# Performance work log

Measured on AMD Instinct MI355X. Metric: run time of the kernel, lower is better.

Reference implementation:

```python
import jax, jax.numpy as jnp
import numpy as np

V = 50000; C0 = 2000; C1 = 10000   # vocab and adaptive-softmax cutoffs
E = 512; H = 1024; B = 32; T = 128
H1 = H // 4; H2 = H // 16           # div_val = 4.0 per source formula
S1 = C1 - C0; S2 = V - C1


def setup_inputs() -> dict:
    key = jax.random.key(0)
    ks = jax.random.split(key, 12)
    # lengths sorted descending, max length == T (required by output.view(b*(T-1),-1))
    lengths = jnp.sort(jax.random.randint(ks[0], (B,), T // 2, T + 1))[::-1]
    lengths = lengths.at[0].set(T).astype(jnp.int64)
    x = jax.random.randint(ks[1], (B, T), 1, V)
    x = jnp.where(jnp.arange(T)[None, :] < lengths[:, None], x, 0).astype(jnp.int64)  # PAD=0 beyond length
    emb = (jax.random.normal(ks[2], (V, E), jnp.float32) * 0.02).at[0].set(0.0)  # padding_idx=0
    w_ih = jax.random.normal(ks[3], (3 * H, E), jnp.float32) * 0.02
    w_hh = jax.random.normal(ks[4], (3 * H, H), jnp.float32) * 0.02
    b_ih = jnp.zeros((3 * H,), jnp.float32)
    b_hh = jnp.zeros((3 * H,), jnp.float32)
    head_w = jax.random.normal(ks[5], (C0 + 2, H), jnp.float32) * 0.02   # shortlist + 2 cluster logits
    p1 = jax.random.normal(ks[6], (H1, H), jnp.float32) * 0.02
    t1 = jax.random.normal(ks[7], (S1, H1), jnp.float32) * 0.02
    p2 = jax.random.normal(ks[8], (H2, H), jnp.float32) * 0.02
    t2 = jax.random.normal(ks[9], (S2, H2), jnp.float32) * 0.02
    hidden = jnp.zeros((1, B, H), jnp.float32)
    return dict(x=x, lengths=lengths, hidden=hidden, emb=emb, w_ih=w_ih, w_hh=w_hh,
                b_ih=b_ih, b_hh=b_hh, head_w=head_w, p1=p1, t1=t1, p2=p2, t2=t2)


def gru_masked(inp, h0, w_ih, w_hh, b_ih, b_hh, lengths):
    """Torch GRU on packed sequence of lengths-1: frozen hidden + zero outputs past length."""
    xp = jnp.einsum('bte,ge->btg', inp, w_ih) + b_ih  # [B, T-1, 3H] input projections

    def step(h, args):
        xpt, t = args
        hp = h @ w_hh.T + b_hh
        xr, xz, xn = jnp.split(xpt, 3, axis=-1)
        hr, hz, hn = jnp.split(hp, 3, axis=-1)
        r = jax.nn.sigmoid(xr + hr)
        z = jax.nn.sigmoid(xz + hz)
        n = jnp.tanh(xn + r * hn)
        h_new = (1.0 - z) * n + z * h
        valid = (t < lengths - 1)[:, None]
        h = jnp.where(valid, h_new, h)          # freeze hidden past sequence end
        y = jnp.where(valid, h, 0.0)            # pad_packed_sequence zero-fills
        return h, y

    steps = jnp.arange(inp.shape[1])
    hT, ys = jax.lax.scan(step, h0, (jnp.swapaxes(xp, 0, 1), steps))
    return jnp.swapaxes(ys, 0, 1), hT  # [B, T-1, H], [B, H]


def adaptive_loss(out, targets, head_w, p1, t1, p2, t2):
    """AdaptiveLogSoftmaxWithLoss: mean NLL over shortlist + 2 tail clusters."""
    N = out.shape[0]
    head_lp = jax.nn.log_softmax(out @ head_w.T, axis=-1)  # [N, C0+2]
    idx = jnp.arange(N)
    lp_short = head_lp[idx, jnp.clip(targets, 0, C0 - 1)]

    def cluster_lp(p, t, ci, lo, size):
        tail_lp = jax.nn.log_softmax((out @ p.T) @ t.T, axis=-1)  # [N, size]
        rel = jnp.clip(targets - lo, 0, size - 1)
        return head_lp[:, C0 + ci] + tail_lp[idx, rel]

    lp1 = cluster_lp(p1, t1, 0, C0, S1)
    lp2 = cluster_lp(p2, t2, 1, C1, S2)
    logp = jnp.where(targets < C0, lp_short, jnp.where(targets < C1, lp1, lp2))
    return -jnp.mean(logp)


def reference(x, lengths, hidden, emb, w_ih, w_hh, b_ih, b_hh, head_w, p1, t1, p2, t2):
    inp = emb[x][:, :T - 1]  # dropout=0.0 -> identity
    ys, hT = gru_masked(inp, hidden[0], w_ih, w_hh, b_ih, b_hh, lengths)
    out = ys.reshape(B * (T - 1), H)
    targets = x[:, 1:].reshape(-1)
    loss = adaptive_loss(out, targets, head_w, p1, t1, p2, t2)
    return loss, hT[None]
```

## Files before the change

kernel.cpp:

```cpp
#include <hip/hip_runtime.h>
#include <math.h>

#define VV   50000
#define CC0  2000
#define CC1  10000
#define ED   512
#define HD   1024
#define BBATCH 32
#define TT   128
#define HH1  256
#define HH2  64
#define SS1  8000
#define SS2  40000
#define NR   4064
#define G3   3072

#define OFF_XP   0ull
#define OFF_YSB  12484608ull
#define OFF_HB   14565376ull
#define OFF_HT   14598144ull
#define OFF_P1B  14630912ull
#define OFF_P2B  15151104ull
#define OFF_WHB  15281152ull
#define OFF_T1B  16306176ull
#define OFF_PP1  17330176ull
#define OFF_PP2  17461248ull
#define OFF_SUM  17494016ull
#define OFF_LOSS (OFF_SUM + 6ull*4064ull)
#define OFF_INT  (OFF_LOSS + 64ull)
#define OFF_WIHB (OFF_INT + 8ull*4064ull)

#define ZERO_N (6*4064 + 64)
#define NBG 64
#define NCONS 192
#define NTILES 608

typedef __attribute__((ext_vector_type(8))) __bf16 bf16x8;
typedef __attribute__((ext_vector_type(4))) float f32x4;
typedef __attribute__((ext_vector_type(4))) unsigned int u32x4;
typedef unsigned long long u64;
typedef unsigned short u16;
struct ull2s { u64 x, y; };

__device__ __forceinline__ u16 f2bf(float f) {
    unsigned u = __builtin_bit_cast(unsigned, f);
    u += 0x7fff + ((u >> 16) & 1);
    return (u16)(u >> 16);
}

__global__ void init_k(const float* __restrict__ hidden, u16* __restrict__ hb0,
                       float* __restrict__ zreg, int* __restrict__ cnt1,
                       int* __restrict__ cnt2, int* __restrict__ bar)
{
    int i = blockIdx.x * 256 + threadIdx.x;
    if (i < BBATCH * HD) hb0[i] = f2bf(hidden[i]);
    int zi = i - BBATCH * HD;
    if (zi >= 0 && zi < ZERO_N) zreg[zi] = 0.f;
    if (zi == ZERO_N) { *cnt1 = 0; *cnt2 = 0; }
    int bi = zi - (ZERO_N + 1);
    if (bi >= 0 && bi < 2048) bar[bi] = 0;
}

__global__ void prep_k(const int* __restrict__ x, int* __restrict__ targets,
                       int* __restrict__ hselc, int* __restrict__ list1,
                       int* __restrict__ list2, int* __restrict__ cnt1, int* __restrict__ cnt2)
{
    int n = blockIdx.x * 256 + threadIdx.x;
    if (n >= NR) return;
    int t = n >> 5, b = n & 31;
    int tgt = x[b * TT + t + 1];
    targets[n] = tgt;
    hselc[n] = (tgt < CC0) ? tgt : ((tgt < CC1) ? CC0 : CC0 + 1);
    if (tgt >= CC0 && tgt < CC1) list1[atomicAdd(cnt1, 1)] = n;
    else if (tgt >= CC1)         list2[atomicAdd(cnt2, 1)] = n;
}

__global__ void cvt_bf16_k(const float* __restrict__ src, u16* __restrict__ dst, int n4)
{
    int i = blockIdx.x * 256 + threadIdx.x;
    if (i >= n4) return;
    float4 f = *(const float4*)(src + 4 * (size_t)i);
    union { u16 h[4]; u64 v; } u;
    u.h[0] = f2bf(f.x); u.h[1] = f2bf(f.y); u.h[2] = f2bf(f.z); u.h[3] = f2bf(f.w);
    *(u64*)&dst[4 * (size_t)i] = u.v;
}

__global__ void cvt_multi_k(const float* __restrict__ s0, u16* __restrict__ d0, int n0,
                            const float* __restrict__ s1, u16* __restrict__ d1, int n1,
                            const float* __restrict__ s2, u16* __restrict__ d2, int n2,
                            const float* __restrict__ s3, u16* __restrict__ d3, int n3,
                            const float* __restrict__ s4, u16* __restrict__ d4, int n4)
{
    int i = blockIdx.x * 256 + threadIdx.x;
    const float* s; u16* d; int off = i;
    if (off < n0) { s = s0; d = d0; }
    else if ((off -= n0) < n1) { s = s1; d = d1; }
    else if ((off -= n1) < n2) { s = s2; d = d2; }
    else if ((off -= n2) < n3) { s = s3; d = d3; }
    else if ((off -= n3) < n4) { s = s4; d = d4; }
    else return;
    float4 f = *(const float4*)(s + 4 * (size_t)off);
    union { u16 h[4]; u64 v; } u;
    u.h[0] = f2bf(f.x); u.h[1] = f2bf(f.y); u.h[2] = f2bf(f.z); u.h[3] = f2bf(f.w);
    *(u64*)&d[4 * (size_t)off] = u.v;
}

__global__ void emb_gather_k(const int* __restrict__ x, const float* __restrict__ emb,
                             u16* __restrict__ embA)
{
    int idx = blockIdx.x * 256 + threadIdx.x;
    if (idx >= NR * 64) return;
    int n = idx >> 6;
    int kk = (idx & 63) << 3;
    int b = n & 31, t = n >> 5;
    int tok = x[b * TT + t];
    const float* ap = emb + (size_t)tok * ED + kk;
    float4 f0 = *(const float4*)ap;
    float4 f1 = *(const float4*)(ap + 4);
    union { u16 h[8]; u32x4 v; } u;
    u.h[0] = f2bf(f0.x); u.h[1] = f2bf(f0.y); u.h[2] = f2bf(f0.z); u.h[3] = f2bf(f0.w);
    u.h[4] = f2bf(f1.x); u.h[5] = f2bf(f1.y); u.h[6] = f2bf(f1.z); u.h[7] = f2bf(f1.w);
    *(u32x4*)&embA[(size_t)n * ED + kk] = u.v;
}

template<int EPI, int BFP32>
__global__ void __launch_bounds__(256)
mfma_gemm_k(const u16* __restrict__ Ab, const void* __restrict__ Bsrc,
            int Mdirect, int N, int K,
            const int* __restrict__ rowmap, const int* __restrict__ cntp,
            u16* __restrict__ outB, int ldo,
            float* __restrict__ gsum, float* __restrict__ gsel,
            const int* __restrict__ selcol, const int* __restrict__ targets, int lo)
{
    const int M = cntp ? *cntp : Mdirect;
    const int rbase = blockIdx.x * 128;
    if (rbase >= M) return;
    const int cbase = blockIdx.y * 128;

    __shared__ u16 As[128 * 40];
    __shared__ u16 Bs[128 * 40];
    __shared__ const u16* aptr[128];
    __shared__ int rown[128];
    __shared__ float redl[128 * 2];

    const int tid = threadIdx.x;
    if (tid < 128) {
        int rid = -1;
        if (rbase + tid < M) rid = rowmap ? rowmap[rbase + tid] : (rbase + tid);
        rown[tid] = rid;
        aptr[tid] = (rid >= 0) ? (Ab + (size_t)rid * K) : nullptr;
    }
    __syncthreads();

    const int lane = tid & 63, wid = tid >> 6;
    const int n16 = lane & 15, quad = lane >> 4;
    const int m0 = (wid >> 1) * 64, n0 = (wid & 1) * 64;
    const int i = tid >> 1, half = tid & 1;

    f32x4 acc[4][4];
#pragma unroll
    for (int a = 0; a < 4; a++)
#pragma unroll
        for (int b = 0; b < 4; b++) acc[a][b] = (f32x4){0.f, 0.f, 0.f, 0.f};

    for (int k0 = 0; k0 < K; k0 += 32) {
        const u16* ap = aptr[i];
        u32x4 a0 = {0,0,0,0}, a1 = a0;
        if (ap) {
            a0 = *(const u32x4*)(ap + k0 + half * 16);
            a1 = *(const u32x4*)(ap + k0 + half * 16 + 8);
        }
        u32x4 b0 = {0,0,0,0}, b1 = b0;
        int c = cbase + i;
        if (c < N) {
            if (BFP32) {
                const float* bp = (const float*)Bsrc + (size_t)c * K + k0 + half * 16;
                float4 f0 = *(const float4*)(bp);
                float4 f1 = *(const float4*)(bp + 4);
                float4 f2 = *(const float4*)(bp + 8);
                float4 f3 = *(const float4*)(bp + 12);
                union { u16 h[16]; u32x4 v[2]; } u;
                u.h[0]=f2bf(f0.x); u.h[1]=f2bf(f0.y); u.h[2]=f2bf(f0.z); u.h[3]=f2bf(f0.w);
                u.h[4]=f2bf(f1.x); u.h[5]=f2bf(f1.y); u.h[6]=f2bf(f1.z); u.h[7]=f2bf(f1.w);
                u.h[8]=f2bf(f2.x); u.h[9]=f2bf(f2.y); u.h[10]=f2bf(f2.z); u.h[11]=f2bf(f2.w);
                u.h[12]=f2bf(f3.x); u.h[13]=f2bf(f3.y); u.h[14]=f2bf(f3.z); u.h[15]=f2bf(f3.w);
                b0 = u.v[0]; b1 = u.v[1];
            } else {
                const u16* bp = (const u16*)Bsrc + (size_t)c * K + k0 + half * 16;
                b0 = *(const u32x4*)(bp);
                b1 = *(const u32x4*)(bp + 8);
            }
        }
        __syncthreads();
        *(u32x4*)&As[i * 40 + half * 16]     = a0;
        *(u32x4*)&As[i * 40 + half * 16 + 8] = a1;
        *(u32x4*)&Bs[i * 40 + half * 16]     = b0;
        *(u32x4*)&Bs[i * 40 + half * 16 + 8] = b1;
        __syncthreads();

        bf16x8 av[4], bv[4];
#pragma unroll
        for (int mi = 0; mi < 4; mi++)
            av[mi] = *(const bf16x8*)&As[(m0 + mi * 16 + n16) * 40 + quad * 8];
#pragma unroll
        for (int ni = 0; ni < 4; ni++)
            bv[ni] = *(const bf16x8*)&Bs[(n0 + ni * 16 + n16) * 40 + quad * 8];
#pragma unroll
        for (int mi = 0; mi < 4; mi++)
#pragma unroll
            for (int ni = 0; ni < 4; ni++)
                acc[mi][ni] = __builtin_amdgcn_mfma_f32_16x16x32_bf16(
                    av[mi], bv[ni], acc[mi][ni], 0, 0, 0);
    }

    __syncthreads();
    if (EPI == 0) {
#pragma unroll
        for (int mi = 0; mi < 4; mi++)
#pragma unroll
            for (int ni = 0; ni < 4; ni++)
#pragma unroll
                for (int r = 0; r < 4; r++) {
                    int row = rbase + m0 + mi * 16 + quad * 4 + r;
                    int col = cbase + n0 + ni * 16 + n16;
                    if (row < M && col < N)
                        outB[(size_t)row * ldo + col] = f2bf(acc[mi][ni][r]);
                }
    } else if (EPI == 3) {
#pragma unroll
        for (int mi = 0; mi < 4; mi++)
#pragma unroll
            for (int ni = 0; ni < 4; ni++)
#pragma unroll
                for (int r = 0; r < 4; r++) {
                    int row = rbase + m0 + mi * 16 + quad * 4 + r;
                    int col = cbase + n0 + ni * 16 + n16;
                    if (row < M && col < N)
                        gsum[(size_t)row * ldo + col] = acc[mi][ni][r] + gsel[col];
                }
    } else {
#pragma unroll
        for (int mi = 0; mi < 4; mi++)
#pragma unroll
            for (int r = 0; r < 4; r++) {
                int lrow = m0 + mi * 16 + quad * 4 + r;
                int nid = rown[lrow];
                float s = 0.f;
                if (nid >= 0) {
                    int sc = (EPI == 1) ? selcol[nid] : (targets[nid] - lo);
#pragma unroll
                    for (int ni = 0; ni < 4; ni++) {
                        int col = cbase + n0 + ni * 16 + n16;
                        if (col < N) {
                            float v = acc[mi][ni][r];
                            s += __expf(v);
                            if (col == sc) gsel[nid] = v;
                        }
                    }
                }
                s += __shfl_xor(s, 1);
                s += __shfl_xor(s, 2);
                s += __shfl_xor(s, 4);
                s += __shfl_xor(s, 8);
                if (n16 == 0) redl[lrow * 2 + (wid & 1)] = s;
            }
        __syncthreads();
        if (tid < 128) {
            int nid = rown[tid];
            if (nid >= 0) atomicAdd(&gsum[nid], redl[tid * 2] + redl[tid * 2 + 1]);
        }
    }
}

__global__ void __launch_bounds__(256, 1)
gru_fused_k(const float* __restrict__ xp, const float* __restrict__ hidden,
            u16* __restrict__ hb0, u16* __restrict__ hb1,
            const float* __restrict__ w_hh, const float* __restrict__ b_hh,
            const int* __restrict__ lengths, u16* __restrict__ ys,
            float* __restrict__ hT, int* __restrict__ flags,
            const u16* __restrict__ whb, const u16* __restrict__ pp1b,
            const u16* __restrict__ pp2b, u16* __restrict__ p1b,
            u16* __restrict__ p2b, float* __restrict__ hsum,
            float* __restrict__ hsel, const int* __restrict__ hselc)
{
    __shared__ u16 Blds[48 * 1032];
    __shared__ u16 As[128 * 40];
    __shared__ u16 Bs[128 * 40];
    __shared__ const u16* aptr[128];
    __shared__ int rown[128];
    __shared__ float redl[128 * 2];

    const int tid = threadIdx.x;
    const int lane = tid & 63;
    const int n16 = lane & 15, quad = lane >> 4;

    if (blockIdx.x < NBG) {
        const int bid = blockIdx.x;
        const int j0 = bid * 16;
        const int wid = tid >> 6;

        for (int idx = tid; idx < 48 * 1024; idx += 256) {
            int r = idx >> 10, k = idx & 1023;
            int g = r >> 4, c = r & 15;
            Blds[r * 1032 + k] = f2bf(w_hh[(size_t)(g * HD + j0 + c) * HD + k]);
        }

        const int col = j0 + n16;
        float bh0 = 0.f, bh1 = 0.f, bh2 = 0.f;
        float hold[4];
        int len[4] = {0, 0, 0, 0};
        if (tid < 128) {
            bh0 = b_hh[col]; bh1 = b_hh[HD + col]; bh2 = b_hh[2 * HD + col];
#pragma unroll
            for (int r = 0; r < 4; r++) {
                int b = wid * 16 + quad * 4 + r;
                len[r] = lengths[b];
                hold[r] = hidden[b * HD + col];
            }
        }
        __syncthreads();

        const int boff = n16 * 1032 + quad * 8;
        const size_t rowoff = (size_t)(wid * 16 + n16) * HD + quad * 8;

        for (int t = 0; t < TT - 1; t++) {
            if (tid < 128) {
                const u16* hb = (t & 1) ? hb1 : hb0;
                u16* hbn = (t & 1) ? hb0 : hb1;

                float xrv[4], xzv[4], xnv[4];
#pragma unroll
                for (int r = 0; r < 4; r++) {
                    int b = wid * 16 + quad * 4 + r;
                    const float* xpt = xp + ((size_t)t * BBATCH + b) * G3 + col;
                    xrv[r] = xpt[0]; xzv[r] = xpt[HD]; xnv[r] = xpt[2 * HD];
                }

                const u16* arow = hb + rowoff;
                u64 apf[64];
#pragma unroll
                for (int ks = 0; ks < 32; ks++) {
                    apf[2*ks]   = __hip_atomic_load((const u64*)(arow + ks*32),
                                      __ATOMIC_RELAXED, __HIP_MEMORY_SCOPE_AGENT);
                    apf[2*ks+1] = __hip_atomic_load((const u64*)(arow + ks*32 + 4),
                                      __ATOMIC_RELAXED, __HIP_MEMORY_SCOPE_AGENT);
                }

                f32x4 acc0 = {0.f, 0.f, 0.f, 0.f}, acc1 = acc0, acc2 = acc0;
#pragma unroll
                for (int ks = 0; ks < 32; ks++) {
                    ull2s av2; av2.x = apf[2*ks]; av2.y = apf[2*ks+1];
                    bf16x8 av = __builtin_bit_cast(bf16x8, av2);
                    bf16x8 b0 = *(const bf16x8*)&Blds[boff + ks*32];
                    bf16x8 b1 = *(const bf16x8*)&Blds[16*1032 + boff + ks*32];
                    bf16x8 b2 = *(const bf16x8*)&Blds[32*1032 + boff + ks*32];
                    acc0 = __builtin_amdgcn_mfma_f32_16x16x32_bf16(av, b0, acc0, 0, 0, 0);
                    acc1 = __builtin_amdgcn_mfma_f32_16x16x32_bf16(av, b1, acc1, 0, 0, 0);
                    acc2 = __builtin_amdgcn_mfma_f32_16x16x32_bf16(av, b2, acc2, 0, 0, 0);
                }

#pragma unroll
                for (int r = 0; r < 4; r++) {
                    int b = wid * 16 + quad * 4 + r;
                    float hr = acc0[r] + bh0, hz = acc1[r] + bh1, hn = acc2[r] + bh2;
                    float rg = 1.f / (1.f + __expf(-(xrv[r] + hr)));
                    float zg = 1.f / (1.f + __expf(-(xzv[r] + hz)));
                    float nv = tanhf(xnv[r] + rg * hn);
                    bool valid = t < (len[r] - 1);
                    float hnew = valid ? (1.f - zg) * nv + zg * hold[r] : hold[r];
                    hold[r] = hnew;
                    __hip_atomic_store(hbn + (size_t)b * HD + col, f2bf(hnew),
                                       __ATOMIC_RELAXED, __HIP_MEMORY_SCOPE_AGENT);
                    __hip_atomic_store(ys + ((size_t)t * BBATCH + b) * HD + col,
                                       f2bf(valid ? hnew : 0.f),
                                       __ATOMIC_RELAXED, __HIP_MEMORY_SCOPE_AGENT);
                    if (t == TT - 2) hT[b * HD + col] = hnew;
                }
            }

            __syncthreads();
            if (tid < 64) {
                if (tid == 0) {
                    __builtin_amdgcn_s_waitcnt(0);
                    __hip_atomic_store(&flags[bid * 32], t + 1, __ATOMIC_RELAXED,
                                       __HIP_MEMORY_SCOPE_AGENT);
                }
                int guard = 0;
                while (__hip_atomic_load(&flags[tid * 32], __ATOMIC_RELAXED,
                                         __HIP_MEMORY_SCOPE_AGENT) < t + 1
                       && guard < (1 << 20)) {
                    __builtin_amdgcn_s_sleep(1);
                    guard++;
                }
            }
            asm volatile("" ::: "memory");
            __syncthreads();
        }
    } else {
        const int wid4 = tid >> 6;
        const int m0 = (wid4 >> 1) * 64, n0 = (wid4 & 1) * 64;
        const int i = tid >> 1, half = tid & 1;
        const int cb = blockIdx.x - NBG;

        for (int g = cb; g < NTILES; g += NCONS) {
            int x, y, N, ldo = 0, epi;
            const u16* Bp; u16* outp = nullptr;
            if (g < 512)      { x = g >> 4;  y = g & 15; N = CC0 + 2; Bp = whb;  epi = 1; }
            else if (g < 576) { int gg = g - 512; x = gg >> 1; y = gg & 1;
                                N = HH1; Bp = pp1b; outp = p1b; ldo = HH1; epi = 0; }
            else              { x = g - 576; y = 0;
                                N = HH2; Bp = pp2b; outp = p2b; ldo = HH2; epi = 0; }
            const int rbase = x * 128, cbase = y * 128;

            int tneed = 4 * x + 4; if (tneed > TT - 1) tneed = TT - 1;
            {
                int guard = 0;
                while (true) {
                    int f = __hip_atomic_load(&flags[lane * 32], __ATOMIC_RELAXED,
                                              __HIP_MEMORY_SCOPE_AGENT);
                    if (__ballot(f >= tneed) == ~0ull) break;
                    if (++guard >= (1 << 20)) break;
                    __builtin_amdgcn_s_sleep(8);
                }
            }
            asm volatile("" ::: "memory");

            __syncthreads();
            if (tid < 128) {
                int rid = (rbase + tid < NR) ? (rbase + tid) : -1;
                rown[tid] = rid;
                aptr[tid] = (rid >= 0) ? (ys + (size_t)rid * HD) : nullptr;
            }
            __syncthreads();

            f32x4 acc[4][4];
#pragma unroll
            for (int a = 0; a < 4; a++)
#pragma unroll
                for (int b = 0; b < 4; b++) acc[a][b] = (f32x4){0.f, 0.f, 0.f, 0.f};

            for (int k0 = 0; k0 < HD; k0 += 32) {
                const u16* ap = aptr[i];
                u64 a0 = 0, a1 = 0, a2 = 0, a3 = 0;
                if (ap) {
                    const u64* p = (const u64*)(ap + k0 + half * 16);
                    a0 = __hip_atomic_load(p,     __ATOMIC_RELAXED, __HIP_MEMORY_SCOPE_AGENT);
                    a1 = __hip_atomic_load(p + 1, __ATOMIC_RELAXED, __HIP_MEMORY_SCOPE_AGENT);
                    a2 = __hip_atomic_load(p + 2, __ATOMIC_RELAXED, __HIP_MEMORY_SCOPE_AGENT);
                    a3 = __hip_atomic_load(p + 3, __ATOMIC_RELAXED, __HIP_MEMORY_SCOPE_AGENT);
                }
                u32x4 b0v = {0,0,0,0}, b1v = b0v;
                int c = cbase + i;
                if (c < N) {
                    const u16* bp = Bp + (size_t)c * HD + k0 + half * 16;
                    b0v = *(const u32x4*)(bp);
                    b1v = *(const u32x4*)(bp + 8);
                }
                __syncthreads();
                *(u64*)&As[i * 40 + half * 16]      = a0;
                *(u64*)&As[i * 40 + half * 16 + 4]  = a1;
                *(u64*)&As[i * 40 + half * 16 + 8]  = a2;
                *(u64*)&As[i * 40 + half * 16 + 12] = a3;
                *(u32x4*)&Bs[i * 40 + half * 16]     = b0v;
                *(u32x4*)&Bs[i * 40 + half * 16 + 8] = b1v;
                __syncthreads();

                bf16x8 av[4], bv[4];
#pragma unroll
                for (int mi = 0; mi < 4; mi++)
                    av[mi] = *(const bf16x8*)&As[(m0 + mi * 16 + n16) * 40 + quad * 8];
#pragma unroll
                for (int ni = 0; ni < 4; ni++)
                    bv[ni] = *(const bf16x8*)&Bs[(n0 + ni * 16 + n16) * 40 + quad * 8];
#pragma unroll
                for (int mi = 0; mi < 4; mi++)
#pragma unroll
                    for (int ni = 0; ni < 4; ni++)
                        acc[mi][ni] = __builtin_amdgcn_mfma_f32_16x16x32_bf16(
                            av[mi], bv[ni], acc[mi][ni], 0, 0, 0);
            }

            __syncthreads();
            if (epi == 0) {
#pragma unroll
                for (int mi = 0; mi < 4; mi++)
#pragma unroll
                    for (int ni = 0; ni < 4; ni++)
#pragma unroll
                        for (int r = 0; r < 4; r++) {
                            int row = rbase + m0 + mi * 16 + quad * 4 + r;
                            int col = cbase + n0 + ni * 16 + n16;
                            if (row < NR && col < N)
                                outp[(size_t)row * ldo + col] = f2bf(acc[mi][ni][r]);
                        }
            } else {
#pragma unroll
                for (int mi = 0; mi < 4; mi++)
#pragma unroll
                    for (int r = 0; r < 4; r++) {
                        int lrow = m0 + mi * 16 + quad * 4 + r;
                        int nid = rown[lrow];
                        float s = 0.f;
                        if (nid >= 0) {
                            int sc = hselc[nid];
#pragma unroll
                            for (int ni = 0; ni < 4; ni++) {
                                int col = cbase + n0 + ni * 16 + n16;
                                if (col < N) {
                                    float v = acc[mi][ni][r];
                                    s += __expf(v);
                                    if (col == sc) hsel[nid] = v;
                                }
                            }
                        }
                        s += __shfl_xor(s, 1);
                        s += __shfl_xor(s, 2);
                        s += __shfl_xor(s, 4);
                        s += __shfl_xor(s, 8);
                        if (n16 == 0) redl[lrow * 2 + (wid4 & 1)] = s;
                    }
                __syncthreads();
                if (tid < 128) {
                    int nid = rown[tid];
                    if (nid >= 0) atomicAdd(&hsum[nid], redl[tid * 2] + redl[tid * 2 + 1]);
                }
            }
        }
    }
}

__global__ void finish_k(const float* __restrict__ hsum, const float* __restrict__ hsel,
                         const float* __restrict__ t1sum, const float* __restrict__ t1sel,
                         const float* __restrict__ t2sum, const float* __restrict__ t2sel,
                         const int* __restrict__ targets, float* __restrict__ losssum)
{
    __shared__ float red[256];
    int n = blockIdx.x * 256 + threadIdx.x;
    float lp = 0.f;
    if (n < NR) {
        lp = hsel[n] - logf(hsum[n]);
        int tgt = targets[n];
        if (tgt >= CC1)      lp += t2sel[n] - logf(t2sum[n]);
        else if (tgt >= CC0) lp += t1sel[n] - logf(t1sum[n]);
    }
    red[threadIdx.x] = lp;
    __syncthreads();
    for (int s = 128; s > 0; s >>= 1) {
        if (threadIdx.x < s) red[threadIdx.x] += red[threadIdx.x + s];
        __syncthreads();
    }
    if (threadIdx.x == 0) atomicAdd(losssum, red[0]);
}

__global__ void out_k(const float* __restrict__ losssum, const float* __restrict__ hT,
                      float* __restrict__ out)
{
    int i = blockIdx.x * 256 + threadIdx.x;
    if (i == 0) out[0] = -losssum[0] / (float)NR;
    if (i < BBATCH * HD) out[1 + i] = hT[i];
}

extern "C" void kernel_launch(void* const* d_in, const int* in_sizes, int n_in,
                              void* d_out, int out_size, void* d_ws, size_t ws_size,
                              hipStream_t stream)
{
    const int*   x       = (const int*)d_in[0];
    const int*   lengths = (const int*)d_in[1];
    const float* hidden  = (const float*)d_in[2];
    const float* emb     = (const float*)d_in[3];
    const float* w_ih    = (const float*)d_in[4];
    const float* w_hh    = (const float*)d_in[5];
    const float* b_ih    = (const float*)d_in[6];
    const float* b_hh    = (const float*)d_in[7];
    const float* head_w  = (const float*)d_in[8];
    const float* p1      = (const float*)d_in[9];
    const float* t1      = (const float*)d_in[10];
    const float* p2      = (const float*)d_in[11];
    const float* t2      = (const float*)d_in[12];

    float* ws = (float*)d_ws;
    float* xp    = ws + OFF_XP;
    u16*   ysb   = (u16*)(ws + OFF_YSB);
    u16*   hb0   = (u16*)(ws + OFF_HB);
    u16*   hb1   = hb0 + BBATCH * HD;
    float* hT    = ws + OFF_HT;
    u16*   p1b   = (u16*)(ws + OFF_P1B);
    u16*   p2b   = (u16*)(ws + OFF_P2B);
    u16*   whb   = (u16*)(ws + OFF_WHB);
    u16*   t1b   = (u16*)(ws + OFF_T1B);
    u16*   pp1b  = (u16*)(ws + OFF_PP1);
    u16*   pp2b  = (u16*)(ws + OFF_PP2);
    float* hsum  = ws + OFF_SUM;
    float* hsel  = hsum + 4064;
    float* t1sum = hsel + 4064;
    float* t1sel = t1sum + 4064;
    float* t2sum = t1sel + 4064;
    float* t2sel = t2sum + 4064;
    float* losss = ws + OFF_LOSS;
    int* ib      = (int*)(ws + OFF_INT);
    int* targets = ib;
    int* hselc   = ib + 4064;
    int* list1   = ib + 2 * 4064;
    int* list2   = ib + 3 * 4064;
    int* cnt1    = ib + 4 * 4064;
    int* cnt2    = cnt1 + 1;
    int* flags   = ib + 5 * 4064;

    u16* embA = (u16*)(ws + OFF_YSB);
    u16* wihb = (u16*)(ws + OFF_WIHB);
    u16* t2b  = (u16*)(ws + OFF_XP);

    float* out = (float*)d_out;

    init_k<<<232, 256, 0, stream>>>(hidden, hb0, hsum, cnt1, cnt2, flags);
    prep_k<<<16, 256, 0, stream>>>(x, targets, hselc, list1, list2, cnt1, cnt2);

    cvt_multi_k<<<(1499648 + 255) / 256, 256, 0, stream>>>(
        w_ih, wihb, 393216,
        head_w, whb, 512512,
        t1, t1b, 512000,
        p1, pp1b, 65536,
        p2, pp2b, 16384);

    emb_gather_k<<<(NR * 64 + 255) / 256, 256, 0, stream>>>(x, emb, embA);
    mfma_gemm_k<3, 0><<<dim3(32, 24), 256, 0, stream>>>(
        embA, wihb, NR, G3, ED, nullptr, nullptr, nullptr, G3,
        xp, (float*)b_ih, nullptr, nullptr, 0);

    gru_fused_k<<<NBG + NCONS, 256, 0, stream>>>(
        xp, hidden, hb0, hb1, w_hh, b_hh, lengths, ysb, hT, flags,
        whb, pp1b, pp2b, p1b, p2b, hsum, hsel, hselc);

    cvt_bf16_k<<<(640000 + 255) / 256, 256, 0, stream>>>(t2, t2b, 640000);

    mfma_gemm_k<2, 0><<<dim3(32, 63), 256, 0, stream>>>(
        p1b, t1b, 0, SS1, HH1, list1, cnt1, nullptr, 0,
        t1sum, t1sel, nullptr, targets, CC0);
    mfma_gemm_k<2, 0><<<dim3(32, 313), 256, 0, stream>>>(
        p2b, t2b, 0, SS2, HH2, list2, cnt2, nullptr, 0,
        t2sum, t2sel, nullptr, targets, CC1);

    finish_k<<<16, 256, 0, stream>>>(hsum, hsel, t1sum, t1sel, t2sum, t2sel,
                                     targets, losss);
    out_k<<<128, 256, 0, stream>>>(losss, hT, out);
}
```

Before: 1.354 ms.

## Fold input-projection GEMM into persistent GRU kernel and merge tail GEMMs

Moves the embedding-by-W_ih input projection GEMM into the consumer blocks of the persistent GRU kernel, which publish completion through an atomic counter. The recurrence blocks wait on that counter before starting, and xp is read with atomic loads. The two tail-cluster GEMM launches are also merged into a single tails_k launch. The aim is to remove launch gaps and let the projection overlap with GRU setup, at the cost of spin-waiting. Because the GRU must wait for the whole projection before it starts, there is little real overlap.

```diff
diff --git a/kernel.cpp b/kernel.cpp
--- a/kernel.cpp
+++ b/kernel.cpp
@@ -33,7 +33,12 @@
 #define ZERO_N (6*4064 + 64)
 #define NBG 64
 #define NCONS 192
-#define NTILES 608
+#define NBARZ 3136
+
+#define G_XP   768
+#define G_HEAD 1280
+#define G_P1   1344
+#define G_TOT  1376
 
 typedef __attribute__((ext_vector_type(8))) __bf16 bf16x8;
 typedef __attribute__((ext_vector_type(4))) float f32x4;
@@ -58,7 +63,7 @@
     if (zi >= 0 && zi < ZERO_N) zreg[zi] = 0.f;
     if (zi == ZERO_N) { *cnt1 = 0; *cnt2 = 0; }
     int bi = zi - (ZERO_N + 1);
-    if (bi >= 0 && bi < 2048) bar[bi] = 0;
+    if (bi >= 0 && bi < NBARZ) bar[bi] = 0;
 }
 
 __global__ void prep_k(const int* __restrict__ x, int* __restrict__ targets,
@@ -123,157 +128,8 @@
     *(u32x4*)&embA[(size_t)n * ED + kk] = u.v;
 }
 
-template<int EPI, int BFP32>
-__global__ void __launch_bounds__(256)
-mfma_gemm_k(const u16* __restrict__ Ab, const void* __restrict__ Bsrc,
-            int Mdirect, int N, int K,
-            const int* __restrict__ rowmap, const int* __restrict__ cntp,
-            u16* __restrict__ outB, int ldo,
-            float* __restrict__ gsum, float* __restrict__ gsel,
-            const int* __restrict__ selcol, const int* __restrict__ targets, int lo)
-{
-    const int M = cntp ? *cntp : Mdirect;
-    const int rbase = blockIdx.x * 128;
-    if (rbase >= M) return;
-    const int cbase = blockIdx.y * 128;
-
-    __shared__ u16 As[128 * 40];
-    __shared__ u16 Bs[128 * 40];
-    __shared__ const u16* aptr[128];
-    __shared__ int rown[128];
-    __shared__ float redl[128 * 2];
-
-    const int tid = threadIdx.x;
-    if (tid < 128) {
-        int rid = -1;
-        if (rbase + tid < M) rid = rowmap ? rowmap[rbase + tid] : (rbase + tid);
-        rown[tid] = rid;
-        aptr[tid] = (rid >= 0) ? (Ab + (size_t)rid * K) : nullptr;
-    }
-    __syncthreads();
-
-    const int lane = tid & 63, wid = tid >> 6;
-    const int n16 = lane & 15, quad = lane >> 4;
-    const int m0 = (wid >> 1) * 64, n0 = (wid & 1) * 64;
-    const int i = tid >> 1, half = tid & 1;
-
-    f32x4 acc[4][4];
-#pragma unroll
-    for (int a = 0; a < 4; a++)
-#pragma unroll
-        for (int b = 0; b < 4; b++) acc[a][b] = (f32x4){0.f, 0.f, 0.f, 0.f};
-
-    for (int k0 = 0; k0 < K; k0 += 32) {
-        const u16* ap = aptr[i];
-        u32x4 a0 = {0,0,0,0}, a1 = a0;
-        if (ap) {
-            a0 = *(const u32x4*)(ap + k0 + half * 16);
-            a1 = *(const u32x4*)(ap + k0 + half * 16 + 8);
-        }
-        u32x4 b0 = {0,0,0,0}, b1 = b0;
-        int c = cbase + i;
-        if (c < N) {
-            if (BFP32) {
-                const float* bp = (const float*)Bsrc + (size_t)c * K + k0 + half * 16;
-                float4 f0 = *(const float4*)(bp);
-                float4 f1 = *(const float4*)(bp + 4);
-                float4 f2 = *(const float4*)(bp + 8);
-                float4 f3 = *(const float4*)(bp + 12);
-                union { u16 h[16]; u32x4 v[2]; } u;
-                u.h[0]=f2bf(f0.x); u.h[1]=f2bf(f0.y); u.h[2]=f2bf(f0.z); u.h[3]=f2bf(f0.w);
-                u.h[4]=f2bf(f1.x); u.h[5]=f2bf(f1.y); u.h[6]=f2bf(f1.z); u.h[7]=f2bf(f1.w);
-                u.h[8]=f2bf(f2.x); u.h[9]=f2bf(f2.y); u.h[10]=f2bf(f2.z); u.h[11]=f2bf(f2.w);
-                u.h[12]=f2bf(f3.x); u.h[13]=f2bf(f3.y); u.h[14]=f2bf(f3.z); u.h[15]=f2bf(f3.w);
-                b0 = u.v[0]; b1 = u.v[1];
-            } else {
-                const u16* bp = (const u16*)Bsrc + (size_t)c * K + k0 + half * 16;
-                b0 = *(const u32x4*)(bp);
-                b1 = *(const u32x4*)(bp + 8);
-            }
-        }
-        __syncthreads();
-        *(u32x4*)&As[i * 40 + half * 16]     = a0;
-        *(u32x4*)&As[i * 40 + half * 16 + 8] = a1;
-        *(u32x4*)&Bs[i * 40 + half * 16]     = b0;
-        *(u32x4*)&Bs[i * 40 + half * 16 + 8] = b1;
-        __syncthreads();
-
-        bf16x8 av[4], bv[4];
-#pragma unroll
-        for (int mi = 0; mi < 4; mi++)
-            av[mi] = *(const bf16x8*)&As[(m0 + mi * 16 + n16) * 40 + quad * 8];
-#pragma unroll
-        for (int ni = 0; ni < 4; ni++)
-            bv[ni] = *(const bf16x8*)&Bs[(n0 + ni * 16 + n16) * 40 + quad * 8];
-#pragma unroll
-        for (int mi = 0; mi < 4; mi++)
-#pragma unroll
-            for (int ni = 0; ni < 4; ni++)
-                acc[mi][ni] = __builtin_amdgcn_mfma_f32_16x16x32_bf16(
-                    av[mi], bv[ni], acc[mi][ni], 0, 0, 0);
-    }
-
-    __syncthreads();
-    if (EPI == 0) {
-#pragma unroll
-        for (int mi = 0; mi < 4; mi++)
-#pragma unroll
-            for (int ni = 0; ni < 4; ni++)
-#pragma unroll
-                for (int r = 0; r < 4; r++) {
-                    int row = rbase + m0 + mi * 16 + quad * 4 + r;
-                    int col = cbase + n0 + ni * 16 + n16;
-                    if (row < M && col < N)
-                        outB[(size_t)row * ldo + col] = f2bf(acc[mi][ni][r]);
-                }
-    } else if (EPI == 3) {
-#pragma unroll
-        for (int mi = 0; mi < 4; mi++)
-#pragma unroll
-            for (int ni = 0; ni < 4; ni++)
-#pragma unroll
-                for (int r = 0; r < 4; r++) {
-                    int row = rbase + m0 + mi * 16 + quad * 4 + r;
-                    int col = cbase + n0 + ni * 16 + n16;
-                    if (row < M && col < N)
-                        gsum[(size_t)row * ldo + col] = acc[mi][ni][r] + gsel[col];
-                }
-    } else {
-#pragma unroll
-        for (int mi = 0; mi < 4; mi++)
-#pragma unroll
-            for (int r = 0; r < 4; r++) {
-                int lrow = m0 + mi * 16 + quad * 4 + r;
-                int nid = rown[lrow];
-                float s = 0.f;
-                if (nid >= 0) {
-                    int sc = (EPI == 1) ? selcol[nid] : (targets[nid] - lo);
-#pragma unroll
-                    for (int ni = 0; ni < 4; ni++) {
-                        int col = cbase + n0 + ni * 16 + n16;
-                        if (col < N) {
-                            float v = acc[mi][ni][r];
-                            s += __expf(v);
-                            if (col == sc) gsel[nid] = v;
-                        }
-                    }
-                }
-                s += __shfl_xor(s, 1);
-                s += __shfl_xor(s, 2);
-                s += __shfl_xor(s, 4);
-                s += __shfl_xor(s, 8);
-                if (n16 == 0) redl[lrow * 2 + (wid & 1)] = s;
-            }
-        __syncthreads();
-        if (tid < 128) {
-            int nid = rown[tid];
-            if (nid >= 0) atomicAdd(&gsum[nid], redl[tid * 2] + redl[tid * 2 + 1]);
-        }
-    }
-}
-
 __global__ void __launch_bounds__(256, 1)
-gru_fused_k(const float* __restrict__ xp, const float* __restrict__ hidden,
+gru_fused_k(float* __restrict__ xp, const float* __restrict__ hidden,
             u16* __restrict__ hb0, u16* __restrict__ hb1,
             const float* __restrict__ w_hh, const float* __restrict__ b_hh,
             const int* __restrict__ lengths, u16* __restrict__ ys,
@@ -281,7 +137,9 @@
             const u16* __restrict__ whb, const u16* __restrict__ pp1b,
             const u16* __restrict__ pp2b, u16* __restrict__ p1b,
             u16* __restrict__ p2b, float* __restrict__ hsum,
-            float* __restrict__ hsel, const int* __restrict__ hselc)
+            float* __restrict__ hsel, const int* __restrict__ hselc,
+            const u16* __restrict__ embA, const u16* __restrict__ wihb,
+            const float* __restrict__ b_ih)
 {
     __shared__ u16 Blds[48 * 1032];
     __shared__ u16 As[128 * 40];
@@ -294,6 +152,8 @@
     const int lane = tid & 63;
     const int n16 = lane & 15, quad = lane >> 4;
 
+    int* xpall = flags + 2048;
+
     if (blockIdx.x < NBG) {
         const int bid = blockIdx.x;
         const int j0 = bid * 16;
@@ -320,6 +180,17 @@
         }
         __syncthreads();
 
+        if (tid == 0) {
+            int guard = 0;
+            while (__hip_atomic_load(xpall, __ATOMIC_RELAXED,
+                                     __HIP_MEMORY_SCOPE_AGENT) < G_XP
+                   && guard < (1 << 20)) {
+                __builtin_amdgcn_s_sleep(8);
+                guard++;
+            }
+        }
+        __syncthreads();
+
         const int boff = n16 * 1032 + quad * 8;
         const size_t rowoff = (size_t)(wid * 16 + n16) * HD + quad * 8;
 
@@ -333,7 +204,12 @@
                 for (int r = 0; r < 4; r++) {
                     int b = wid * 16 + quad * 4 + r;
                     const float* xpt = xp + ((size_t)t * BBATCH + b) * G3 + col;
-                    xrv[r] = xpt[0]; xzv[r] = xpt[HD]; xnv[r] = xpt[2 * HD];
+                    xrv[r] = __hip_atomic_load(xpt, __ATOMIC_RELAXED,
+                                               __HIP_MEMORY_SCOPE_AGENT);
+                    xzv[r] = __hip_atomic_load(xpt + HD, __ATOMIC_RELAXED,
+                                               __HIP_MEMORY_SCOPE_AGENT);
+                    xnv[r] = __hip_atomic_load(xpt + 2 * HD, __ATOMIC_RELAXED,
+                                               __HIP_MEMORY_SCOPE_AGENT);
                 }
 
                 const u16* arow = hb + rowoff;
@@ -402,18 +278,22 @@
         const int i = tid >> 1, half = tid & 1;
         const int cb = blockIdx.x - NBG;
 
-        for (int g = cb; g < NTILES; g += NCONS) {
-            int x, y, N, ldo = 0, epi;
-            const u16* Bp; u16* outp = nullptr;
-            if (g < 512)      { x = g >> 4;  y = g & 15; N = CC0 + 2; Bp = whb;  epi = 1; }
-            else if (g < 576) { int gg = g - 512; x = gg >> 1; y = gg & 1;
-                                N = HH1; Bp = pp1b; outp = p1b; ldo = HH1; epi = 0; }
-            else              { x = g - 576; y = 0;
-                                N = HH2; Bp = pp2b; outp = p2b; ldo = HH2; epi = 0; }
+        for (int g = cb; g < G_TOT; g += NCONS) {
+            int x, y, N, K, type;
+            const u16* Ap; const u16* Bp;
+            u16* outp = nullptr; int ldo = 0;
+            if (g < G_XP)       { type = 5; x = g / 24; y = g - x * 24;
+                                  N = G3; K = ED; Ap = embA; Bp = wihb; }
+            else if (g < G_HEAD){ type = 0; int j = g - G_XP; x = j >> 4; y = j & 15;
+                                  N = CC0 + 2; K = HD; Ap = ys; Bp = whb; }
+            else if (g < G_P1)  { type = 1; int j = g - G_HEAD; x = j >> 1; y = j & 1;
+                                  N = HH1; K = HD; Ap = ys; Bp = pp1b; outp = p1b; ldo = HH1; }
+            else                { type = 2; x = g - G_P1; y = 0;
+                                  N = HH2; K = HD; Ap = ys; Bp = pp2b; outp = p2b; ldo = HH2; }
             const int rbase = x * 128, cbase = y * 128;
 
-            int tneed = 4 * x + 4; if (tneed > TT - 1) tneed = TT - 1;
-            {
+            if (type != 5) {
+                int tneed = 4 * x + 4; if (tneed > TT - 1) tneed = TT - 1;
                 int guard = 0;
                 while (true) {
                     int f = __hip_atomic_load(&flags[lane * 32], __ATOMIC_RELAXED,
@@ -429,7 +309,7 @@
             if (tid < 128) {
                 int rid = (rbase + tid < NR) ? (rbase + tid) : -1;
                 rown[tid] = rid;
-                aptr[tid] = (rid >= 0) ? (ys + (size_t)rid * HD) : nullptr;
+                aptr[tid] = (rid >= 0) ? (Ap + (size_t)rid * K) : nullptr;
             }
             __syncthreads();
 
@@ -439,7 +319,7 @@
 #pragma unroll
                 for (int b = 0; b < 4; b++) acc[a][b] = (f32x4){0.f, 0.f, 0.f, 0.f};
 
-            for (int k0 = 0; k0 < HD; k0 += 32) {
+            for (int k0 = 0; k0 < K; k0 += 32) {
                 const u16* ap = aptr[i];
                 u64 a0 = 0, a1 = 0, a2 = 0, a3 = 0;
                 if (ap) {
@@ -452,7 +332,7 @@
                 u32x4 b0v = {0,0,0,0}, b1v = b0v;
                 int c = cbase + i;
                 if (c < N) {
-                    const u16* bp = Bp + (size_t)c * HD + k0 + half * 16;
+                    const u16* bp = Bp + (size_t)c * K + k0 + half * 16;
                     b0v = *(const u32x4*)(bp);
                     b1v = *(const u32x4*)(bp + 8);
                 }
@@ -481,7 +361,27 @@
             }
 
             __syncthreads();
-            if (epi == 0) {
+            if (type == 5) {
+#pragma unroll
+                for (int mi = 0; mi < 4; mi++)
+#pragma unroll
+                    for (int ni = 0; ni < 4; ni++)
+#pragma unroll
+                        for (int r = 0; r < 4; r++) {
+                            int row = rbase + m0 + mi * 16 + quad * 4 + r;
+                            int col = cbase + n0 + ni * 16 + n16;
+                            if (row < NR && col < N)
+                                __hip_atomic_store(xp + (size_t)row * G3 + col,
+                                                   acc[mi][ni][r] + b_ih[col],
+                                                   __ATOMIC_RELAXED, __HIP_MEMORY_SCOPE_AGENT);
+                        }
+                __syncthreads();
+                if (tid == 0) {
+                    __builtin_amdgcn_s_waitcnt(0);
+                    __hip_atomic_fetch_add(xpall, 1, __ATOMIC_RELAXED,
+                                           __HIP_MEMORY_SCOPE_AGENT);
+                }
+            } else if (type == 1 || type == 2) {
 #pragma unroll
                 for (int mi = 0; mi < 4; mi++)
 #pragma unroll
@@ -526,6 +426,121 @@
                 }
             }
         }
+    }
+}
+
+__global__ void __launch_bounds__(256)
+tails_k(const u16* __restrict__ p1b, const u16* __restrict__ t1b,
+        const int* __restrict__ list1, const int* __restrict__ cnt1,
+        float* __restrict__ t1sum, float* __restrict__ t1sel,
+        const u16* __restrict__ p2b, const u16* __restrict__ t2b,
+        const int* __restrict__ list2, const int* __restrict__ cnt2,
+        float* __restrict__ t2sum, float* __restrict__ t2sel,
+        const int* __restrict__ targets)
+{
+    int yy = blockIdx.y;
+    const u16* Ab; const u16* Bb; const int* rowmap; const int* cntp;
+    float *gsum, *gsel; int N, K, lo;
+    if (yy < 63) { Ab = p1b; Bb = t1b; rowmap = list1; cntp = cnt1;
+                   gsum = t1sum; gsel = t1sel; N = SS1; K = HH1; lo = CC0; }
+    else { yy -= 63; Ab = p2b; Bb = t2b; rowmap = list2; cntp = cnt2;
+           gsum = t2sum; gsel = t2sel; N = SS2; K = HH2; lo = CC1; }
+    const int M = *cntp;
+    const int rbase = blockIdx.x * 128;
+    if (rbase >= M) return;
+    const int cbase = yy * 128;
+
+    __shared__ u16 As[128 * 40];
+    __shared__ u16 Bs[128 * 40];
+    __shared__ const u16* aptr[128];
+    __shared__ int rown[128];
+    __shared__ float redl[128 * 2];
+
+    const int tid = threadIdx.x;
+    if (tid < 128) {
+        int rid = (rbase + tid < M) ? rowmap[rbase + tid] : -1;
+        rown[tid] = rid;
+        aptr[tid] = (rid >= 0) ? (Ab + (size_t)rid * K) : nullptr;
+    }
+    __syncthreads();
+
+    const int lane = tid & 63, wid = tid >> 6;
+    const int n16 = lane & 15, quad = lane >> 4;
+    const int m0 = (wid >> 1) * 64, n0 = (wid & 1) * 64;
+    const int i = tid >> 1, half = tid & 1;
+
+    f32x4 acc[4][4];
+#pragma unroll
+    for (int a = 0; a < 4; a++)
+#pragma unroll
+        for (int b = 0; b < 4; b++) acc[a][b] = (f32x4){0.f, 0.f, 0.f, 0.f};
+
+    for (int k0 = 0; k0 < K; k0 += 32) {
+        const u16* ap = aptr[i];
+        u32x4 a0 = {0,0,0,0}, a1 = a0;
+        if (ap) {
+            a0 = *(const u32x4*)(ap + k0 + half * 16);
+            a1 = *(const u32x4*)(ap + k0 + half * 16 + 8);
+        }
+        u32x4 b0 = {0,0,0,0}, b1 = b0;
+        int c = cbase + i;
+        if (c < N) {
+            const u16* bp = Bb + (size_t)c * K + k0 + half * 16;
+            b0 = *(const u32x4*)(bp);
+            b1 = *(const u32x4*)(bp + 8);
+        }
+        __syncthreads();
+        *(u32x4*)&As[i * 40 + half * 16]     = a0;
+        *(u32x4*)&As[i * 40 + half * 16 + 8] = a1;
+        *(u32x4*)&Bs[i * 40 + half * 16]     = b0;
+        *(u32x4*)&Bs[i * 40 + half * 16 + 8] = b1;
+        __syncthreads();
+
+        bf16x8 av[4], bv[4];
+#pragma unroll
+        for (int mi = 0; mi < 4; mi++)
+            av[mi] = *(const bf16x8*)&As[(m0 + mi * 16 + n16) * 40 + quad * 8];
+#pragma unroll
+        for (int ni = 0; ni < 4; ni++)
+            bv[ni] = *(const bf16x8*)&Bs[(n0 + ni * 16 + n16) * 40 + quad * 8];
+#pragma unroll
+        for (int mi = 0; mi < 4; mi++)
+#pragma unroll
+            for (int ni = 0; ni < 4; ni++)
+                acc[mi][ni] = __builtin_amdgcn_mfma_f32_16x16x32_bf16(
+                    av[mi], bv[ni], acc[mi][ni], 0, 0, 0);
+    }
+
+    __syncthreads();
+#pragma unroll
+    for (int mi = 0; mi < 4; mi++)
+#pragma unroll
+        for (int r = 0; r < 4; r++) {
+            int lrow = m0 + mi * 16 + quad * 4 + r;
+            int nid = rown[lrow];
+            float s = 0.f;
+            if (nid >= 0) {
+                int sc = targets[nid] - lo;
+#pragma unroll
+                for (int ni = 0; ni < 4; ni++) {
+                    int col = cbase + n0 + ni * 16 + n16;
+                    if (col < N) {
+                        float v = acc[mi][ni][r];
+                        s += __expf(v);
+                        if (col == sc) gsel[nid] = v;
+                    }
+                }
+            }
+            s += __shfl_xor(s, 1);
+            s += __shfl_xor(s, 2);
+            s += __shfl_xor(s, 4);
+            s += __shfl_xor(s, 8);
+            if (n16 == 0) redl[lrow * 2 + (wid & 1)] = s;
+        }
+    __syncthreads();
+    if (tid < 128) {
+        int nid = rown[tid];
+        if (nid >= 0) atomicAdd(&gsum[nid], redl[tid * 2] + redl[tid * 2 + 1]);
     }
 }
 
@@ -612,7 +627,7 @@
 
     float* out = (float*)d_out;
 
-    init_k<<<232, 256, 0, stream>>>(hidden, hb0, hsum, cnt1, cnt2, flags);
+    init_k<<<240, 256, 0, stream>>>(hidden, hb0, hsum, cnt1, cnt2, flags);
     prep_k<<<16, 256, 0, stream>>>(x, targets, hselc, list1, list2, cnt1, cnt2);
 
     cvt_multi_k<<<(1499648 + 255) / 256, 256, 0, stream>>>(
@@ -623,22 +638,17 @@
         p2, pp2b, 16384);
 
     emb_gather_k<<<(NR * 64 + 255) / 256, 256, 0, stream>>>(x, emb, embA);
-    mfma_gemm_k<3, 0><<<dim3(32, 24), 256, 0, stream>>>(
-        embA, wihb, NR, G3, ED, nullptr, nullptr, nullptr, G3,
-        xp, (float*)b_ih, nullptr, nullptr, 0);
 
     gru_fused_k<<<NBG + NCONS, 256, 0, stream>>>(
         xp, hidden, hb0, hb1, w_hh, b_hh, lengths, ysb, hT, flags,
-        whb, pp1b, pp2b, p1b, p2b, hsum, hsel, hselc);
+        whb, pp1b, pp2b, p1b, p2b, hsum, hsel, hselc,
+        embA, wihb, b_ih);
 
     cvt_bf16_k<<<(640000 + 255) / 256, 256, 0, stream>>>(t2, t2b, 640000);
 
-    mfma_gemm_k<2, 0><<<dim3(32, 63), 256, 0, stream>>>(
-        p1b, t1b, 0, SS1, HH1, list1, cnt1, nullptr, 0,
-        t1sum, t1sel, nullptr, targets, CC0);
-    mfma_gemm_k<2, 0><<<dim3(32, 313), 256, 0, stream>>>(
-        p2b, t2b, 0, SS2, HH2, list2, cnt2, nullptr, 0,
-        t2sum, t2sel, nullptr, targets, CC1);
+    tails_k<<<dim3(32, 376), 256, 0, stream>>>(
+        p1b, t1b, list1, cnt1, t1sum, t1sel,
+        p2b, t2b, list2, cnt2, t2sum, t2sel, targets);
 
     finish_k<<<16, 256, 0, stream>>>(hsum, hsel, t1sum, t1sel, t2sum, t2sel,
                                      targets, losss);
```

Result: slower. 1.446 ms (+6.8%).
